# Kernel tuning notes

Hardware: AMD Instinct MI355X
Metric: run time of the kernel (lower is better)

The kernel has to match this reference:

```python
import jax, jax.numpy as jnp
import numpy as np

C = 64   # in_channels
KS = 3   # kernel_size


def _wconv(p, W1, b1, W2, b2, W3, b3):
    # 1x1 conv stack: 3 -> 64 -> 256 -> C*KS*KS, ReLU between
    h = jax.nn.relu(jnp.einsum('oc,bchw->bohw', W1, p) + b1[None, :, None, None])
    h = jax.nn.relu(jnp.einsum('oc,bchw->bohw', W2, h) + b2[None, :, None, None])
    h = jnp.einsum('oc,bchw->bohw', W3, h) + b3[None, :, None, None]
    return h  # [1, C*KS*KS, ho, wo]


def setup_inputs() -> dict:
    key = jax.random.key(0)
    k = jax.random.split(key, 8)
    bs, hi, wi = 2, 128, 128
    ho, wo = 512, 512
    x = jax.random.normal(k[0], (bs, C, hi, wi), jnp.float32)
    poseMap = jax.random.normal(k[1], (1, 3, ho, wo), jnp.float32)
    interMapY = jax.random.randint(k[2], (ho, wo), 0, hi)
    interMapX = jax.random.randint(k[3], (ho, wo), 0, wi)
    W1 = jax.random.normal(k[4], (64, 3), jnp.float32) * 0.1
    b1 = jnp.zeros((64,), jnp.float32)
    W2 = jax.random.normal(k[5], (256, 64), jnp.float32) * 0.05
    b2 = jnp.zeros((256,), jnp.float32)
    W3 = jax.random.normal(k[6], (C * KS * KS, 256), jnp.float32) * 0.05
    b3 = jnp.zeros((C * KS * KS,), jnp.float32)
    return {'x': x, 'poseMap': poseMap, 'W1': W1, 'b1': b1, 'W2': W2, 'b2': b2,
            'W3': W3, 'b3': b3, 'interMapY': interMapY, 'interMapX': interMapX}


def reference(x, poseMap, W1, b1, W2, b2, W3, b3, interMapY, interMapX):
    bs, c, hi, wi = x.shape
    ho, wo = interMapY.shape
    # kernel prediction branch (poseMap is detached in the original)
    w = _wconv(jax.lax.stop_gradient(poseMap), W1, b1, W2, b2, W3, b3)
    w = w.reshape(C, KS * KS, ho, wo)
    sw = jax.nn.softmax(w, axis=1)  # softmax over the KS*KS taps
    # unfold(x, KS, padding=KS//2) tap k corresponds to xp[:, :, i + k//KS, j + k%KS]
    pad = KS // 2
    xp = jnp.pad(x, ((0, 0), (0, 0), (pad, pad), (pad, pad)))
    out = jnp.zeros((bs, C, ho, wo), x.dtype)
    for k in range(KS * KS):  # fixed small loop over taps; fuses gather+weight+reduce
        dy, dx = k // KS, k % KS
        g = xp[:, :, interMapY + dy, interMapX + dx]  # [bs, C, ho, wo] paired gather
        out = out + g * sw[None, :, k]  # sw[:, k] -> [C, ho, wo]
    return out
```

## Files before the change

### kernel.cpp

```cpp
#include <hip/hip_runtime.h>
#include <math.h>

#define HO 512
#define WO 512
#define HI 128
#define WI 128
#define CC 64
#define BS 2
#define NPX 64
#define NT 256

#define W2P_ELEMS (16 * 2 * 64 * 8)
#define W3P_ELEMS (36 * 8 * 64 * 8)
#define TOTALW    (W2P_ELEMS + W3P_ELEMS)
#define XT_ELEM_OFF TOTALW
#define NBORDER4  16512

typedef __attribute__((ext_vector_type(8))) short short8;
typedef __attribute__((ext_vector_type(4))) short short4v;
typedef __attribute__((ext_vector_type(4))) float float4v;
typedef __attribute__((ext_vector_type(2))) float float2v;

__device__ __forceinline__ unsigned short f2bf(float f) {
    unsigned u = __builtin_bit_cast(unsigned, f);
    unsigned r = (u + 0x7FFFu + ((u >> 16) & 1u)) >> 16;
    return (unsigned short)r;
}

__global__ void prepack_all(const float* __restrict__ x,
                            const float* __restrict__ W2,
                            const float* __restrict__ W3,
                            unsigned short* __restrict__ wsp,
                            float* __restrict__ xt) {
    const int tid = blockIdx.x * blockDim.x + threadIdx.x;
    if (tid < 262144) {
        const int pos = tid & 16383;
        const int g   = tid >> 14;
        const int h = pos >> 7, w = pos & 127;
        const float* src = x + pos;
        float a0[4], a1[4];
        #pragma unroll
        for (int j = 0; j < 4; ++j) a0[j] = src[(size_t)(g * 4 + j) * (HI * WI)];
        #pragma unroll
        for (int j = 0; j < 4; ++j) a1[j] = src[(size_t)(CC + g * 4 + j) * (HI * WI)];
        float* dst = xt + ((h + 1) * 130 + (w + 1)) * 128 + g * 8;
        *(float4v*)dst       = (float4v){a0[0], a1[0], a0[1], a1[1]};
        *(float4v*)(dst + 4) = (float4v){a0[2], a1[2], a0[3], a1[3]};
        return;
    }
    const int idx = tid - 262144;
    if (idx < W2P_ELEMS) {
        int j = idx & 7, lane = (idx >> 3) & 63, rest = idx >> 9;
        int ks = rest & 1, nt = rest >> 1;
        int n = nt * 16 + (lane & 15);
        int k = ks * 32 + (lane >> 4) * 8 + j;
        wsp[idx] = f2bf(W2[n * 64 + k]);
    } else if (idx < TOTALW) {
        int i2 = idx - W2P_ELEMS;
        int j = i2 & 7, lane = (i2 >> 3) & 63, rest = i2 >> 9;
        int ks = rest & 7, nt = rest >> 3;
        int tap = nt >> 2, ct = nt & 3;
        int row = (ct * 16 + (lane & 15)) * 9 + tap;
        int k = ks * 32 + (lane >> 4) * 8 + j;
        wsp[idx] = f2bf(W3[row * 256 + k]);
    } else if (idx < TOTALW + NBORDER4) {
        int a = idx - TOTALW;
        int cell;
        if (a < 2 * 130 * 32) {
            int r = a / (130 * 32);
            int rest = a - r * (130 * 32);
            cell = (r * 129) * 130 + (rest >> 5);
            a = rest;
        } else {
            int a2 = a - 2 * 130 * 32;
            int h = 1 + (a2 >> 6);
            int rest = a2 & 63;
            cell = h * 130 + (rest >> 5) * 129;
            a = rest;
        }
        float4v z = {0.f, 0.f, 0.f, 0.f};
        *(float4v*)(xt + (size_t)cell * 128 + (a & 31) * 4) = z;
    }
}

__global__ __launch_bounds__(NT, 3)
void fused_main(const float* __restrict__ xt, const float* __restrict__ pose,
                const float* __restrict__ W1, const float* __restrict__ b1,
                const float* __restrict__ b2, const float* __restrict__ b3,
                const int* __restrict__ iY, const int* __restrict__ iX,
                const unsigned short* __restrict__ wsp,
                float* __restrict__ out)
{
    __shared__ char smem[33792 + 17408 + 768 + 512];
    unsigned short (*sH2)[264] = (unsigned short (*)[264])&smem[0];
    unsigned short (*sH1)[72]  = (unsigned short (*)[72])&smem[33792];
    float (*sOut)[2][16][68]   = (float (*)[2][16][68])&smem[33792];
    float (*sP)[NPX]           = (float (*)[NPX])&smem[51200];
    int* sIY                   = (int*)&smem[51968];
    int* sIX                   = (int*)&smem[52224];

    const int t = threadIdx.x;
    const int pixBase = blockIdx.x * NPX;
    const int y  = pixBase / WO;
    const int x0 = pixBase % WO;

    if (t < 192) sP[t >> 6][t & 63] = pose[(t >> 6) * (HO * WO) + pixBase + (t & 63)];
    if (t < 64) sIY[t] = iY[pixBase + t];
    else if (t < 128) sIX[t - 64] = iX[pixBase + t - 64];
    __syncthreads();

    {
        const int p  = t & 63;
        const int og = t >> 6;
        const float p0 = sP[0][p], p1 = sP[1][p], p2 = sP[2][p];
        #pragma unroll
        for (int i = 0; i < 16; i += 2) {
            const int o = og * 16 + i;
            float a0 = fmaf(W1[o * 3 + 2], p2, fmaf(W1[o * 3 + 1], p1, fmaf(W1[o * 3 + 0], p0, b1[o])));
            float a1 = fmaf(W1[o * 3 + 5], p2, fmaf(W1[o * 3 + 4], p1, fmaf(W1[o * 3 + 3], p0, b1[o + 1])));
            a0 = fmaxf(a0, 0.f); a1 = fmaxf(a1, 0.f);
            unsigned pack = (unsigned)f2bf(a0) | ((unsigned)f2bf(a1) << 16);
            *(unsigned*)&sH1[p][o] = pack;
        }
    }
    __syncthreads();

    const int wv = t >> 6, l = t & 63, lm = l & 15, lq = l >> 4;
    const int m0 = wv * 16;

    {
        short8 a0 = *(const short8*)&sH1[m0 + lm][0  + lq * 8];
        short8 a1 = *(const short8*)&sH1[m0 + lm][32 + lq * 8];
        const short8* w2f = (const short8*)wsp;
        #pragma unroll 4
        for (int kc = 0; kc < 8; ++kc) {
            const int ntE = 2 * kc, ntO = 2 * kc + 1;
            float4v aE = {0.f, 0.f, 0.f, 0.f}, aO = {0.f, 0.f, 0.f, 0.f};
            short8 e0 = w2f[(ntE * 2 + 0) * 64 + l];
            short8 e1 = w2f[(ntE * 2 + 1) * 64 + l];
            short8 o0 = w2f[(ntO * 2 + 0) * 64 + l];
            short8 o1 = w2f[(ntO * 2 + 1) * 64 + l];
            aE = __builtin_amdgcn_mfma_f32_16x16x32_bf16(e0, a0, aE, 0, 0, 0);
            aE = __builtin_amdgcn_mfma_f32_16x16x32_bf16(e1, a1, aE, 0, 0, 0);
            aO = __builtin_amdgcn_mfma_f32_16x16x32_bf16(o0, a0, aO, 0, 0, 0);
            aO = __builtin_amdgcn_mfma_f32_16x16x32_bf16(o1, a1, aO, 0, 0, 0);
            const float4v bE = *(const float4v*)(b2 + ntE * 16 + lq * 4);
            const float4v bO = *(const float4v*)(b2 + ntO * 16 + lq * 4);
            short4v hE, hO;
            #pragma unroll
            for (int r = 0; r < 4; ++r) {
                hE[r] = (short)f2bf(fmaxf(aE[r] + bE[r], 0.f));
                hO[r] = (short)f2bf(fmaxf(aO[r] + bO[r], 0.f));
            }
            *(short4v*)&sH2[m0 + lm][kc * 32 + lq * 4]      = hE;
            *(short4v*)&sH2[m0 + lm][kc * 32 + 16 + lq * 4] = hO;
        }
    }
    __syncthreads();

    int pbase[4];
    #pragma unroll
    for (int r = 0; r < 4; ++r) {
        const int p = m0 + lq * 4 + r;
        pbase[r] = ((sIY[p] + 1) * 130 + (sIX[p] + 1)) * 128;
    }
    const int koff[9] = {-131 * 128, -130 * 128, -129 * 128,
                         -1 * 128,   0,          1 * 128,
                         129 * 128,  130 * 128,  131 * 128};
    const short8* w3f = (const short8*)(wsp + W2P_ELEMS);

    for (int ct = 0; ct < 4; ++ct) {
        float4v accs[9];
        #pragma unroll
        for (int tap = 0; tap < 9; ++tap) accs[tap] = (float4v){0.f, 0.f, 0.f, 0.f};

        #pragma unroll 2
        for (int ks = 0; ks < 8; ++ks) {
            short8 a = *(const short8*)&sH2[m0 + lm][ks * 32 + lq * 8];
            #pragma unroll
            for (int tap = 0; tap < 9; ++tap) {
                short8 b = w3f[(((tap << 2) | ct) * 8 + ks) * 64 + l];
                accs[tap] = __builtin_amdgcn_mfma_f32_16x16x32_bf16(a, b, accs[tap], 0, 0, 0);
            }
        }

        const int c = ct * 16 + lm;
        float bv[9];
        #pragma unroll
        for (int tap = 0; tap < 9; ++tap) bv[tap] = b3[c * 9 + tap];

        float ob0[4], ob1[4];
        #pragma unroll
        for (int r = 0; r < 4; ++r) {
            float lg[9];
            #pragma unroll
            for (int tap = 0; tap < 9; ++tap) lg[tap] = accs[tap][r] + bv[tap];
            float mx = lg[0];
            #pragma unroll
            for (int tap = 1; tap < 9; ++tap) mx = fmaxf(mx, lg[tap]);
            const float* xb = xt + pbase[r] + 2 * c;
            float s = 0.f, o0 = 0.f, o1 = 0.f;
            #pragma unroll
            for (int tap = 0; tap < 9; ++tap) {
                const float ev = __expf(lg[tap] - mx);
                const float2v gg = *(const float2v*)(xb + koff[tap]);
                s += ev;
                o0 = fmaf(ev, gg[0], o0);
                o1 = fmaf(ev, gg[1], o1);
            }
            const float inv = 1.f / s;
            ob0[r] = o0 * inv;
            ob1[r] = o1 * inv;
        }

        float (*so)[16][68] = sOut[ct & 1];
        *(float4v*)&so[0][lm][m0 + lq * 4] = (float4v){ob0[0], ob0[1], ob0[2], ob0[3]};
        *(float4v*)&so[1][lm][m0 + lq * 4] = (float4v){ob1[0], ob1[1], ob1[2], ob1[3]};
        __syncthreads();

        const int row = t >> 3;
        const int b   = row >> 4, ch = row & 15;
        const int seg = (t & 7) * 8;
        float4v v0 = *(float4v*)&so[b][ch][seg];
        float4v v1 = *(float4v*)&so[b][ch][seg + 4];
        float* op = out + (((size_t)(b * CC + ct * 16 + ch) * HO) + y) * WO + x0 + seg;
        *(float4v*)op = v0;
        *(float4v*)(op + 4) = v1;
    }
}

extern "C" void kernel_launch(void* const* d_in, const int* in_sizes, int n_in,
                              void* d_out, int out_size, void* d_ws, size_t ws_size,
                              hipStream_t stream) {
    const float* x    = (const float*)d_in[0];
    const float* pose = (const float*)d_in[1];
    const float* W1   = (const float*)d_in[2];
    const float* b1   = (const float*)d_in[3];
    const float* W2   = (const float*)d_in[4];
    const float* b2   = (const float*)d_in[5];
    const float* W3   = (const float*)d_in[6];
    const float* b3   = (const float*)d_in[7];
    const int*   iY   = (const int*)d_in[8];
    const int*   iX   = (const int*)d_in[9];
    float* out = (float*)d_out;
    unsigned short* wsp = (unsigned short*)d_ws;
    float* xt = (float*)((char*)d_ws + (size_t)XT_ELEM_OFF * sizeof(unsigned short));

    prepack_all<<<2048, NT, 0, stream>>>(x, W2, W3, wsp, xt);

    const int nblocks = (HO * WO) / NPX;
    fused_main<<<nblocks, NT, 0, stream>>>(
        xt, pose, W1, b1, b2, b3, iY, iX, wsp, out);
}
```

Baseline: 399.5 us.

## Alias sH1 into sH2, drop output staging, write results directly from registers

Layer-2 MFMA operands are swapped so each wave keeps its 16 pixels' data in registers. That lets sH1 share LDS with sH2 after one early barrier, cutting shared memory by roughly a third, which could raise occupancy. The shared-memory output staging buffer and its per-channel-tile barrier are removed, and each lane writes its 4 consecutive pixels as float4 straight to global memory. In exchange, global stores are less coalesced (16-byte chunks scattered across channels), and the sH2 writes become scalar bf16 stores with likely bank conflicts.

```diff
diff --git a/kernel.cpp b/kernel.cpp
--- a/kernel.cpp
+++ b/kernel.cpp
@@ -17,7 +17,6 @@
 #define NBORDER4  16512
 
 typedef __attribute__((ext_vector_type(8))) short short8;
-typedef __attribute__((ext_vector_type(4))) short short4v;
 typedef __attribute__((ext_vector_type(4))) float float4v;
 typedef __attribute__((ext_vector_type(2))) float float2v;
 
@@ -91,13 +90,12 @@
                 const unsigned short* __restrict__ wsp,
                 float* __restrict__ out)
 {
-    __shared__ char smem[33792 + 17408 + 768 + 512];
+    __shared__ char smem[33792 + 768 + 512];
     unsigned short (*sH2)[264] = (unsigned short (*)[264])&smem[0];
-    unsigned short (*sH1)[72]  = (unsigned short (*)[72])&smem[33792];
-    float (*sOut)[2][16][68]   = (float (*)[2][16][68])&smem[33792];
-    float (*sP)[NPX]           = (float (*)[NPX])&smem[51200];
-    int* sIY                   = (int*)&smem[51968];
-    int* sIX                   = (int*)&smem[52224];
+    unsigned short (*sH1)[72]  = (unsigned short (*)[72])&smem[0];
+    float (*sP)[NPX]           = (float (*)[NPX])&smem[33792];
+    int* sIY                   = (int*)&smem[34560];
+    int* sIX                   = (int*)&smem[34816];
 
     const int t = threadIdx.x;
     const int pixBase = blockIdx.x * NPX;
@@ -128,35 +126,25 @@
     const int wv = t >> 6, l = t & 63, lm = l & 15, lq = l >> 4;
     const int m0 = wv * 16;
 
+    short8 a0 = *(const short8*)&sH1[m0 + lm][0  + lq * 8];
+    short8 a1 = *(const short8*)&sH1[m0 + lm][32 + lq * 8];
+    __syncthreads();
+
     {
-        short8 a0 = *(const short8*)&sH1[m0 + lm][0  + lq * 8];
-        short8 a1 = *(const short8*)&sH1[m0 + lm][32 + lq * 8];
         const short8* w2f = (const short8*)wsp;
         #pragma unroll 4
-        for (int kc = 0; kc < 8; ++kc) {
-            const int ntE = 2 * kc, ntO = 2 * kc + 1;
-            float4v aE = {0.f, 0.f, 0.f, 0.f}, aO = {0.f, 0.f, 0.f, 0.f};
-            short8 e0 = w2f[(ntE * 2 + 0) * 64 + l];
-            short8 e1 = w2f[(ntE * 2 + 1) * 64 + l];
-            short8 o0 = w2f[(ntO * 2 + 0) * 64 + l];
-            short8 o1 = w2f[(ntO * 2 + 1) * 64 + l];
-            aE = __builtin_amdgcn_mfma_f32_16x16x32_bf16(e0, a0, aE, 0, 0, 0);
-            aE = __builtin_amdgcn_mfma_f32_16x16x32_bf16(e1, a1, aE, 0, 0, 0);
-            aO = __builtin_amdgcn_mfma_f32_16x16x32_bf16(o0, a0, aO, 0, 0, 0);
-            aO = __builtin_amdgcn_mfma_f32_16x16x32_bf16(o1, a1, aO, 0, 0, 0);
-            const float4v bE = *(const float4v*)(b2 + ntE * 16 + lq * 4);
-            const float4v bO = *(const float4v*)(b2 + ntO * 16 + lq * 4);
-            short4v hE, hO;
-            #pragma unroll
-            for (int r = 0; r < 4; ++r) {
-                hE[r] = (short)f2bf(fmaxf(aE[r] + bE[r], 0.f));
-                hO[r] = (short)f2bf(fmaxf(aO[r] + bO[r], 0.f));
-            }
-            *(short4v*)&sH2[m0 + lm][kc * 32 + lq * 4]      = hE;
-            *(short4v*)&sH2[m0 + lm][kc * 32 + 16 + lq * 4] = hO;
-        }
-    }
-    __syncthreads();
+        for (int nt = 0; nt < 16; ++nt) {
+            float4v acc = {0.f, 0.f, 0.f, 0.f};
+            short8 bf0 = w2f[(nt * 2 + 0) * 64 + l];
+            short8 bf1 = w2f[(nt * 2 + 1) * 64 + l];
+            acc = __builtin_amdgcn_mfma_f32_16x16x32_bf16(a0, bf0, acc, 0, 0, 0);
+            acc = __builtin_amdgcn_mfma_f32_16x16x32_bf16(a1, bf1, acc, 0, 0, 0);
+            const float bv = b2[nt * 16 + lm];
+            #pragma unroll
+            for (int r = 0; r < 4; ++r)
+                sH2[m0 + lq * 4 + r][nt * 16 + lm] = f2bf(fmaxf(acc[r] + bv, 0.f));
+        }
+    }
 
     int pbase[4];
     #pragma unroll
@@ -213,19 +201,11 @@
             ob1[r] = o1 * inv;
         }
 
-        float (*so)[16][68] = sOut[ct & 1];
-        *(float4v*)&so[0][lm][m0 + lq * 4] = (float4v){ob0[0], ob0[1], ob0[2], ob0[3]};
-        *(float4v*)&so[1][lm][m0 + lq * 4] = (float4v){ob1[0], ob1[1], ob1[2], ob1[3]};
-        __syncthreads();
-
-        const int row = t >> 3;
-        const int b   = row >> 4, ch = row & 15;
-        const int seg = (t & 7) * 8;
-        float4v v0 = *(float4v*)&so[b][ch][seg];
-        float4v v1 = *(float4v*)&so[b][ch][seg + 4];
-        float* op = out + (((size_t)(b * CC + ct * 16 + ch) * HO) + y) * WO + x0 + seg;
-        *(float4v*)op = v0;
-        *(float4v*)(op + 4) = v1;
+        const int px = x0 + m0 + lq * 4;
+        float* op0 = out + ((size_t)c * HO + y) * WO + px;
+        float* op1 = op0 + (size_t)CC * HO * WO;
+        *(float4v*)op0 = (float4v){ob0[0], ob0[1], ob0[2], ob0[3]};
+        *(float4v*)op1 = (float4v){ob1[0], ob1[1], ob1[2], ob1[3]};
     }
 }
 
```

Result: no change. 405.3 us (+1.4%).
